# Kernel tuning notes

Hardware: AMD Instinct MI355X
Metric: run time of the kernel (lower is better)

## Reference

```python
import jax, jax.numpy as jnp
import numpy as np


def conv1x1(x, W, b):
    # 1x1 conv == channel mixing: [O,C] x [B,C,H,W] -> [B,O,H,W]
    return jnp.einsum('oc,bchw->bohw', W, x) + b[None, :, None, None]


def _fmm(x, x_th, Wk_rgb, bk_rgb, Wk_th, bk_th, Wv_rgb, bv_rgb, Wv_th, bv_th,
         gamma_rgb, gamma_th, gamma2_rgb, gamma2_th):
    b, c, w, h = x.shape
    n = w * h
    x_k    = conv1x1(x,    Wk_rgb, bk_rgb).reshape(b, c, n)
    x_th_k = conv1x1(x_th, Wk_th,  bk_th ).reshape(b, c, n)
    x_v    = conv1x1(x,    Wv_rgb, bv_rgb).reshape(b, c, n)
    x_v_th = conv1x1(x_th, Wv_th,  bv_th ).reshape(b, c, n)

    # spatial attention: sim[b, n, m] = x_th_k^T @ x_k, softmax over m
    sim = jax.nn.softmax(jnp.einsum('bcn,bcm->bnm', x_th_k, x_k), axis=-1)
    x_1    = jnp.einsum('bcn,bnm->bcm', x_v,    sim).reshape(b, c, w, h)
    x_th_1 = jnp.einsum('bcn,bnm->bcm', x_v_th, sim).reshape(b, c, w, h)
    x_1    = x_1 * gamma_rgb + x
    x_th_1 = x_th_1 * gamma_th + x_th

    # channel attention with max-subtraction (note: uses value projections, not x_1)
    energy = jnp.einsum('bcn,bdn->bcd', x_v_th, x_v)  # [b, c, c]
    sim_c = jax.nn.softmax(jnp.max(energy, axis=-1, keepdims=True) - energy, axis=-1)
    x_2    = jnp.einsum('bcd,bdn->bcn', sim_c, x_v   ).reshape(b, c, w, h)
    x_th_2 = jnp.einsum('bcd,bdn->bcn', sim_c, x_v_th).reshape(b, c, w, h)
    x_2    = gamma2_rgb * x_2    + x_1
    x_th_2 = gamma2_th  * x_th_2 + x_th_1
    return x_2, x_th_2


def setup_inputs() -> dict:
    key = jax.random.key(0)
    ks = jax.random.split(key, 12)
    b, c, w, h = 4, 256, 64, 64
    scale = 1.0 / np.sqrt(c)
    f32 = jnp.float32
    d = {
        'x':    jax.random.normal(ks[0], (b, c, w, h), f32),
        'x_th': jax.random.normal(ks[1], (b, c, w, h), f32),
        'Wk_rgb': jax.random.normal(ks[2], (c, c), f32) * scale,
        'bk_rgb': jax.random.normal(ks[3], (c,), f32) * 0.01,
        'Wk_th':  jax.random.normal(ks[4], (c, c), f32) * scale,
        'bk_th':  jax.random.normal(ks[5], (c,), f32) * 0.01,
        'Wv_rgb': jax.random.normal(ks[6], (c, c), f32) * scale,
        'bv_rgb': jax.random.normal(ks[7], (c,), f32) * 0.01,
        'Wv_th':  jax.random.normal(ks[8], (c, c), f32) * scale,
        'bv_th':  jax.random.normal(ks[9], (c,), f32) * 0.01,
        # gammas init to 0 in the original; use small nonzero so both branches are exercised
        'gamma_rgb':  jnp.full((1,), 0.5, f32),
        'gamma_th':   jnp.full((1,), 0.4, f32),
        'gamma2_rgb': jnp.full((1,), 0.3, f32),
        'gamma2_th':  jnp.full((1,), 0.2, f32),
    }
    return d


def reference(x, x_th, Wk_rgb, bk_rgb, Wk_th, bk_th, Wv_rgb, bv_rgb, Wv_th, bv_th,
              gamma_rgb, gamma_th, gamma2_rgb, gamma2_th):
    return _fmm(x, x_th, Wk_rgb, bk_rgb, Wk_th, bk_th, Wv_rgb, bv_rgb, Wv_th, bv_th,
                gamma_rgb, gamma_th, gamma2_rgb, gamma2_th)
```

## Files before the change

### kernel.cpp

```cpp
#include <hip/hip_runtime.h>

typedef unsigned short u16;
typedef unsigned int u32;
typedef __attribute__((ext_vector_type(8))) _Float16 f16x8;
typedef __attribute__((ext_vector_type(4))) float f32x4;

#define DEVINL __device__ __forceinline__
#define LOG2E 1.44269504f

DEVINL u16 f2h_u(float f) { _Float16 h = (_Float16)f; return __builtin_bit_cast(unsigned short, h); }
DEVINL float h2f_u(u16 h) { return (float)__builtin_bit_cast(_Float16, h); }
DEVINL float ex2(float x) { return __builtin_amdgcn_exp2f(x); }

DEVINL f16x8 ldfrag(const u16* p) {
    int4 d = *(const int4*)p;
    return __builtin_bit_cast(f16x8, d);
}

DEVINL void glds16(const u16* g, u16* l) {
    __builtin_amdgcn_global_load_lds(
        (const __attribute__((address_space(1))) unsigned int*)g,
        (__attribute__((address_space(3))) unsigned int*)l, 16, 0, 0);
}

#define CFENCE  asm volatile("" ::: "memory")
#define VMCNT8  asm volatile("s_waitcnt vmcnt(8)" ::: "memory")
#define VMCNT0  asm volatile("s_waitcnt vmcnt(0)" ::: "memory")
#define LGKM0   asm volatile("s_waitcnt lgkmcnt(0)" ::: "memory")

static const long CN  = 256L * 4096L;
static const long PtE = 4096L * 4096L;

DEVINL void gemm_core(const u16* __restrict__ Ag, int lda,
                      const u16* __restrict__ Bg, int ldb,
                      int kOff, int kLen, u16* As, u16* Bs, f32x4 (&acc)[4][4])
{
    int tid = threadIdx.x;
    int lane = tid & 63, w = tid >> 6;
    int wr = w >> 1, wc = w & 1;
    int kg = lane >> 4, rl = lane & 15;
    int l8 = lane >> 3, c8 = lane & 7;

    int srow = w * 32 + l8;
    int scol = (c8 ^ l8) * 8;
    const u16* aS = Ag + (size_t)srow * lda + kOff + scol;
    const u16* bS = Bg + (size_t)srow * ldb + kOff + scol;
    int dOff = w * 2048;

    int rl7 = rl & 7;
    int e0 = (kg ^ rl7) * 8;
    int e1 = e0 ^ 32;
    int aRow = (wr * 64 + rl) * 64;
    int bRow = (wc * 64 + rl) * 64;

    int nt = kLen >> 6;
#pragma unroll
    for (int q = 0; q < 4; ++q) {
        glds16(aS + (size_t)q * 8 * lda, As + dOff + q * 512);
        glds16(bS + (size_t)q * 8 * ldb, Bs + dOff + q * 512);
    }
#pragma unroll
    for (int q = 0; q < 4; ++q) {
        glds16(aS + (size_t)q * 8 * lda + 64, As + 8192 + dOff + q * 512);
        glds16(bS + (size_t)q * 8 * ldb + 64, Bs + 8192 + dOff + q * 512);
    }

    for (int t = 0; t < nt; ++t) {
        const u16* Ab = As + (t & 1) * 8192;
        const u16* Bb = Bs + (t & 1) * 8192;
        if (t + 1 < nt) { VMCNT8; } else { VMCNT0; }
        __builtin_amdgcn_s_barrier();
        CFENCE;
        f16x8 a0[4], b0[4], a1[4], b1[4];
#pragma unroll
        for (int i = 0; i < 4; ++i) a0[i] = ldfrag(&Ab[aRow + i * 1024 + e0]);
#pragma unroll
        for (int i = 0; i < 4; ++i) b0[i] = ldfrag(&Bb[bRow + i * 1024 + e0]);
#pragma unroll
        for (int i = 0; i < 4; ++i) a1[i] = ldfrag(&Ab[aRow + i * 1024 + e1]);
#pragma unroll
        for (int i = 0; i < 4; ++i) b1[i] = ldfrag(&Bb[bRow + i * 1024 + e1]);
        __builtin_amdgcn_s_setprio(1);
#pragma unroll
        for (int i = 0; i < 4; ++i)
#pragma unroll
            for (int j = 0; j < 4; ++j)
                acc[i][j] = __builtin_amdgcn_mfma_f32_16x16x32_f16(a0[i], b0[j], acc[i][j], 0, 0, 0);
#pragma unroll
        for (int i = 0; i < 4; ++i)
#pragma unroll
            for (int j = 0; j < 4; ++j)
                acc[i][j] = __builtin_amdgcn_mfma_f32_16x16x32_f16(a1[i], b1[j], acc[i][j], 0, 0, 0);
        __builtin_amdgcn_s_setprio(0);
        LGKM0;
        __builtin_amdgcn_s_barrier();
        CFENCE;
        if (t + 2 < nt) {
            const u16* aN = aS + (size_t)(t + 2) * 64;
            const u16* bN = bS + (size_t)(t + 2) * 64;
            u16* Ad = As + (t & 1) * 8192 + dOff;
            u16* Bd = Bs + (t & 1) * 8192 + dOff;
#pragma unroll
            for (int q = 0; q < 4; ++q) {
                glds16(aN + (size_t)q * 8 * lda, Ad + q * 512);
                glds16(bN + (size_t)q * 8 * ldb, Bd + q * 512);
            }
        }
    }
}

DEVINL void epi_f32_apply(f32x4 (&acc)[4][4], u16* AsRaw, int rowBase, int colBase,
                          float gamma, const float* __restrict__ src,
                          float* __restrict__ out)
{
    int tid = threadIdx.x;
    int lane = tid & 63, w = tid >> 6;
    int wr = w >> 1, wc = w & 1, kg = lane >> 4, rl = lane & 15;
    int rrow = lane & 15, rcg = lane >> 4;
    float* slab = (float*)AsRaw + w * 320;
#pragma unroll
    for (int i = 0; i < 4; ++i) {
        int row0 = rowBase + wr * 64 + i * 16;
#pragma unroll
        for (int j = 0; j < 4; ++j) {
            int col0 = colBase + wc * 64 + j * 16;
            f32x4 v = acc[i][j];
#pragma unroll
            for (int r = 0; r < 4; ++r) slab[(kg * 4 + r) * 20 + rl] = v[r];
            LGKM0;
            float4 vv = *(const float4*)(slab + rrow * 20 + rcg * 4);
            CFENCE;
            size_t o = (size_t)(row0 + rrow) * 4096 + col0 + rcg * 4;
            float4 sv = *(const float4*)(src + o);
            float4 ov;
            ov.x = gamma * vv.x + sv.x;
            ov.y = gamma * vv.y + sv.y;
            ov.z = gamma * vv.z + sv.z;
            ov.w = gamma * vv.w + sv.w;
            *(float4*)(out + o) = ov;
        }
    }
}

DEVINL void epi_f16_bias(f32x4 (&acc)[4][4], u16* AsRaw, int rowBase, int colBase,
                         int ldo, const float* __restrict__ bias, u16* __restrict__ out)
{
    int tid = threadIdx.x;
    int lane = tid & 63, w = tid >> 6;
    int wr = w >> 1, wc = w & 1, kg = lane >> 4, rl = lane & 15;
    int rrow = lane & 15, rcg = lane >> 4;
    float* slab = (float*)AsRaw + w * 320;
#pragma unroll
    for (int i = 0; i < 4; ++i) {
        int row0 = rowBase + wr * 64 + i * 16;
#pragma unroll
        for (int j = 0; j < 4; ++j) {
            int col0 = colBase + wc * 64 + j * 16;
            f32x4 v = acc[i][j];
#pragma unroll
            for (int r = 0; r < 4; ++r) slab[(kg * 4 + r) * 20 + rl] = v[r];
            LGKM0;
            float4 vv = *(const float4*)(slab + rrow * 20 + rcg * 4);
            CFENCE;
            float4 bb = *(const float4*)(bias + col0 + rcg * 4);
            u32 lo = (u32)f2h_u(vv.x + bb.x) | ((u32)f2h_u(vv.y + bb.y) << 16);
            u32 hi = (u32)f2h_u(vv.z + bb.z) | ((u32)f2h_u(vv.w + bb.w) << 16);
            uint2 pk; pk.x = lo; pk.y = hi;
            *(uint2*)(out + (size_t)(row0 + rrow) * ldo + col0 + rcg * 4) = pk;
        }
    }
}

DEVINL void mergeMS(float& m, float& s, float om, float os) {
    float nm = fmaxf(m, om);
    s = s * ex2((m - nm) * LOG2E) + os * ex2((om - nm) * LOG2E);
    m = nm;
}

__launch_bounds__(256, 2)
__global__ void st_gemm(const u16* __restrict__ Kt, const u16* __restrict__ Ktth,
                        u16* __restrict__ StH,
                        float* __restrict__ pmax, float* __restrict__ psum)
{
    __shared__ __align__(16) u16 As[2 * 8192];
    __shared__ __align__(16) u16 Bs[2 * 8192];
    int P = blockIdx.x;
    int L = (P & 7) * 512 + (P >> 3);
    int b = L >> 10, yb = (L >> 5) & 31, xb = L & 31;
    const u16* A = Kt   + (long)b * CN + (size_t)yb * 128 * 256;
    const u16* B = Ktth + (long)b * CN + (size_t)xb * 128 * 256;
    u16* out = StH + (long)b * PtE;
    int rowBase = yb * 128, colBase = xb * 128;

    f32x4 acc[4][4];
#pragma unroll
    for (int i = 0; i < 4; ++i)
#pragma unroll
        for (int j = 0; j < 4; ++j) acc[i][j] = (f32x4){0.f, 0.f, 0.f, 0.f};

    gemm_core(A, 256, B, 256, 0, 256, As, Bs, acc);

    int lane = threadIdx.x & 63, w = threadIdx.x >> 6;
    int wr = w >> 1, wc = w & 1, kg = lane >> 4, rl = lane & 15;
    int rrow = lane & 15, rcg = lane >> 4;
    float* slab = (float*)As + w * 320;

    float vr[4][4][4];
#pragma unroll
    for (int i = 0; i < 4; ++i) {
        int row0 = rowBase + wr * 64 + i * 16;
#pragma unroll
        for (int j = 0; j < 4; ++j) {
            int col0 = colBase + wc * 64 + j * 16;
            f32x4 v = acc[i][j];
#pragma unroll
            for (int r = 0; r < 4; ++r) {
                float xr = h2f_u(f2h_u(v[r]));
                vr[i][j][r] = xr;
                slab[(kg * 4 + r) * 20 + rl] = xr;
            }
            LGKM0;
            float4 vv = *(const float4*)(slab + rrow * 20 + rcg * 4);
            CFENCE;
            u32 lo = (u32)f2h_u(vv.x) | ((u32)f2h_u(vv.y) << 16);
            u32 hi = (u32)f2h_u(vv.z) | ((u32)f2h_u(vv.w) << 16);
            uint2 pk; pk.x = lo; pk.y = hi;
            *(uint2*)(out + (size_t)(row0 + rrow) * 4096 + col0 + rcg * 4) = pk;
        }
    }
    float tm[4], ts[4];
#pragma unroll
    for (int j = 0; j < 4; ++j) {
        float m = vr[0][j][0];
#pragma unroll
        for (int i = 0; i < 4; ++i)
#pragma unroll
            for (int r = 0; r < 4; ++r) m = fmaxf(m, vr[i][j][r]);
        float mk = m * LOG2E, s = 0.f;
#pragma unroll
        for (int i = 0; i < 4; ++i)
#pragma unroll
            for (int r = 0; r < 4; ++r) s += ex2(fmaf(vr[i][j][r], LOG2E, -mk));
        tm[j] = m; ts[j] = s;
    }
#pragma unroll
    for (int j = 0; j < 4; ++j) {
        mergeMS(tm[j], ts[j], __shfl_xor(tm[j], 16, 64), __shfl_xor(ts[j], 16, 64));
        mergeMS(tm[j], ts[j], __shfl_xor(tm[j], 32, 64), __shfl_xor(ts[j], 32, 64));
    }
    float* red = (float*)Bs;
    __syncthreads();
    if (wr == 1 && lane < 16) {
#pragma unroll
        for (int j = 0; j < 4; ++j) {
            red[((wc * 4 + j) * 16 + rl) * 2 + 0] = tm[j];
            red[((wc * 4 + j) * 16 + rl) * 2 + 1] = ts[j];
        }
    }
    __syncthreads();
    if (wr == 0 && lane < 16) {
#pragma unroll
        for (int j = 0; j < 4; ++j) {
            mergeMS(tm[j], ts[j], red[((wc * 4 + j) * 16 + rl) * 2 + 0],
                                  red[((wc * 4 + j) * 16 + rl) * 2 + 1]);
            int col = colBase + wc * 64 + j * 16 + rl;
            long idx = ((long)b * 32 + yb) * 4096 + col;
            pmax[idx] = tm[j];
            psum[idx] = ts[j];
        }
    }
}

__global__ void stats_combine(const float* __restrict__ pmax, const float* __restrict__ psum,
                              float* __restrict__ cmK, float* __restrict__ crcp)
{
    int b = blockIdx.y;
    int col = blockIdx.x * 256 + threadIdx.x;
    const float* pm = pmax + (long)b * 32 * 4096 + col;
    const float* ps = psum + (long)b * 32 * 4096 + col;
    float m = -3.0e38f, s = 0.f;
    for (int i = 0; i < 32; ++i) mergeMS(m, s, pm[i * 4096], ps[i * 4096]);
    cmK[b * 4096 + col] = m * LOG2E;
    crcp[b * 4096 + col] = 1.f / s;
}

__global__ void pt8_kernel(u16* St, const float* __restrict__ cmK,
                           const float* __restrict__ crcp)
{
    int b = blockIdx.z;
    St += (long)b * PtE;
    cmK += b * 4096; crcp += b * 4096;
    int m = blockIdx.y;
    int c0 = (blockIdx.x * 256 + threadIdx.x) * 8;
    size_t o = (size_t)m * 4096 + c0;
    f16x8 hv = __builtin_bit_cast(f16x8, *(const int4*)(St + o));
    union { u16 q[8]; int4 v; } pk;
#pragma unroll
    for (int j = 0; j < 8; ++j)
        pk.q[j] = f2h_u(ex2(fmaf((float)hv[j], LOG2E, -cmK[c0 + j])) * crcp[c0 + j]);
    *(int4*)(St + o) = pk.v;
}

__launch_bounds__(256, 2)
__global__ void pv_gemm(const u16* __restrict__ V2, const u16* __restrict__ Pt,
                        const float* __restrict__ g0p, const float* __restrict__ g1p,
                        const float* __restrict__ src0, const float* __restrict__ src1,
                        float* __restrict__ out0, float* __restrict__ out1)
{
    __shared__ __align__(16) u16 As[2 * 8192];
    __shared__ __align__(16) u16 Bs[2 * 8192];
    int P = blockIdx.x;
    int L = (P & 7) * 64 + (P >> 3);
    int b = L >> 7, n = (L >> 2) & 31, y = (L >> 1) & 1, t = L & 1;
    const u16* A = V2 + ((long)b * 2 + t) * CN;
    const u16* B = Pt + (long)b * PtE;
    int rowBase = y * 128, colBase = n * 128;

    f32x4 acc[4][4];
#pragma unroll
    for (int i = 0; i < 4; ++i)
#pragma unroll
        for (int j = 0; j < 4; ++j) acc[i][j] = (f32x4){0.f, 0.f, 0.f, 0.f};

    gemm_core(A + (size_t)rowBase * 4096, 4096, B + (size_t)colBase * 4096, 4096,
              0, 4096, As, Bs, acc);

    float gamma = t ? *g1p : *g0p;
    const float* src = (t ? src1 : src0) + (long)b * CN;
    float* out = (t ? out1 : out0) + (long)b * CN;
    epi_f32_apply(acc, As, rowBase, colBase, gamma, src, out);
}

__launch_bounds__(256, 2)
__global__ void gemm_splitk(const u16* __restrict__ A, int lda, long sAz,
                            const u16* __restrict__ B, int ldb, long sBz,
                            int splitK, int zshift,
                            float* __restrict__ outf, int ldo, long sOz)
{
    __shared__ __align__(16) u16 As[2 * 8192];
    __shared__ __align__(16) u16 Bs[2 * 8192];
    int z = blockIdx.z;
    int bq = z >> zshift, s = z & ((1 << zshift) - 1);
    int kOff = s * splitK;
    A += sAz * bq; B += sBz * bq;
    long zo = sOz * bq;
    int rowBase = blockIdx.y * 128, colBase = blockIdx.x * 128;
    f32x4 acc[4][4];
#pragma unroll
    for (int i = 0; i < 4; ++i)
#pragma unroll
        for (int j = 0; j < 4; ++j) acc[i][j] = (f32x4){0.f, 0.f, 0.f, 0.f};

    gemm_core(A + (size_t)rowBase * lda, lda, B + (size_t)colBase * ldb, ldb, kOff, splitK, As, Bs, acc);

    int lane = threadIdx.x & 63, w = threadIdx.x >> 6;
    int wr = w >> 1, wc = w & 1, kg = lane >> 4, rl = lane & 15;
#pragma unroll
    for (int i = 0; i < 4; ++i) {
        int row0 = rowBase + wr * 64 + i * 16 + kg * 4;
#pragma unroll
        for (int j = 0; j < 4; ++j) {
            int col = colBase + wc * 64 + j * 16 + rl;
            f32x4 v = acc[i][j];
#pragma unroll
            for (int r = 0; r < 4; ++r)
                atomicAdd(&outf[zo + (size_t)(row0 + r) * ldo + col], v[r]);
        }
    }
}

__launch_bounds__(256, 2)
__global__ void proj_all(const u16* __restrict__ xT, const u16* __restrict__ xthT,
                         const u16* __restrict__ wts,
                         const float* __restrict__ b0, const float* __restrict__ b1,
                         const float* __restrict__ b2, const float* __restrict__ b3,
                         u16* o0, u16* o1, u16* o2, u16* o3)
{
    __shared__ __align__(16) u16 As[2 * 8192];
    __shared__ __align__(16) u16 Bs[2 * 8192];
    int z = blockIdx.z, b = z >> 2, t = z & 3;
    const u16* A = ((t & 1) ? xthT : xT) + (long)b * CN;
    const u16* B = wts + t * 65536;
    u16* out = t == 0 ? o0 + (long)b * CN : t == 1 ? o1 + (long)b * CN
             : t == 2 ? o2 + (long)b * 2 * CN : o3 + (long)b * 2 * CN;
    int rowBase = blockIdx.y * 128, colBase = blockIdx.x * 128;
    f32x4 acc[4][4];
#pragma unroll
    for (int i = 0; i < 4; ++i)
#pragma unroll
        for (int j = 0; j < 4; ++j) acc[i][j] = (f32x4){0.f, 0.f, 0.f, 0.f};

    gemm_core(A + (size_t)rowBase * 256, 256, B + (size_t)colBase * 256, 256, 0, 256, As, Bs, acc);

    const float* bias = t == 0 ? b0 : t == 1 ? b1 : t == 2 ? b2 : b3;
    epi_f16_bias(acc, As, rowBase, colBase, 256, bias, out);
}

__launch_bounds__(256, 2)
__global__ void ch_gemm(const u16* __restrict__ simcb, const u16* __restrict__ Vt2,
                        const float* __restrict__ g0p, const float* __restrict__ g1p,
                        const float* __restrict__ src0, const float* __restrict__ src1,
                        float* __restrict__ out0, float* __restrict__ out1)
{
    __shared__ __align__(16) u16 As[2 * 8192];
    __shared__ __align__(16) u16 Bs[2 * 8192];
    int P = blockIdx.x;
    int L = (P & 7) * 64 + (P >> 3);
    int b = L >> 7, t = (L >> 6) & 1, n = (L >> 1) & 31, y = L & 1;
    const u16* A = simcb + (long)b * 65536;
    const u16* B = Vt2 + ((long)b * 2 + t) * CN;
    int rowBase = y * 128, colBase = n * 128;

    f32x4 acc[4][4];
#pragma unroll
    for (int i = 0; i < 4; ++i)
#pragma unroll
        for (int j = 0; j < 4; ++j) acc[i][j] = (f32x4){0.f, 0.f, 0.f, 0.f};

    gemm_core(A + (size_t)rowBase * 256, 256, B + (size_t)colBase * 256, 256, 0, 256, As, Bs, acc);

    float gamma = t ? *g1p : *g0p;
    const float* src = (t ? src1 : src0) + (long)b * CN;
    float* out = (t ? out1 : out0) + (long)b * CN;
    epi_f32_apply(acc, As, rowBase, colBase, gamma, src, out);
}

__global__ void tr_f32_h2(const float* __restrict__ in0, const float* __restrict__ in1,
                          u16* __restrict__ out0, u16* __restrict__ out1)
{
    int z = blockIdx.z, b = z & 3;
    const float* in = ((z >> 2) ? in1 : in0) + (long)b * CN;
    u16* out = ((z >> 2) ? out1 : out0) + (long)b * CN;
    __shared__ u16 s[64 * 65];
    int tx = threadIdx.x & 63, tw = threadIdx.x >> 6;
    int r0 = blockIdx.y * 64, c0 = blockIdx.x * 64;
#pragma unroll
    for (int p = 0; p < 16; ++p) {
        int r = tw + p * 4;
        s[tx * 65 + r] = f2h_u(in[(size_t)(r0 + r) * 4096 + c0 + tx]);
    }
    __syncthreads();
#pragma unroll
    for (int p = 0; p < 16; ++p) {
        int rr = tw + p * 4;
        out[(size_t)(c0 + rr) * 256 + r0 + tx] = s[rr * 65 + tx];
    }
}

__global__ void tr_h_h(const u16* __restrict__ in, u16* __restrict__ out,
                       int R, int NC_, long sIn, long sOut)
{
    in += (long)blockIdx.z * sIn; out += (long)blockIdx.z * sOut;
    __shared__ u16 s[64 * 65];
    int tx = threadIdx.x & 63, tw = threadIdx.x >> 6;
    int r0 = blockIdx.y * 64, c0 = blockIdx.x * 64;
#pragma unroll
    for (int p = 0; p < 16; ++p) {
        int r = tw + p * 4;
        s[tx * 65 + r] = in[(size_t)(r0 + r) * NC_ + c0 + tx];
    }
    __syncthreads();
#pragma unroll
    for (int p = 0; p < 16; ++p) {
        int rr = tw + p * 4;
        out[(size_t)(c0 + rr) * R + r0 + tx] = s[rr * 65 + tx];
    }
}

__global__ void cvt_w_kernel(const float* __restrict__ w0, const float* __restrict__ w1,
                             const float* __restrict__ w2, const float* __restrict__ w3,
                             u16* __restrict__ out)
{
    int i = blockIdx.x * 256 + threadIdx.x;
    const float* w = (i < 65536) ? w0 : (i < 131072) ? w1 : (i < 196608) ? w2 : w3;
    out[i] = f2h_u(w[i & 65535]);
}

DEVINL float blockReduce(float v, int op) {
    __shared__ float s[4];
#pragma unroll
    for (int o = 32; o; o >>= 1) {
        float t = __shfl_xor(v, o, 64);
        v = op ? (v + t) : fmaxf(v, t);
    }
    __syncthreads();
    if ((threadIdx.x & 63) == 0) s[threadIdx.x >> 6] = v;
    __syncthreads();
    return op ? (s[0] + s[1] + s[2] + s[3]) : fmaxf(fmaxf(s[0], s[1]), fmaxf(s[2], s[3]));
}

__global__ void simc_kernel(const float* __restrict__ E, u16* __restrict__ simc)
{
    int bb = blockIdx.y;
    const float* Eb = E + bb * 65536;
    u16* sc = simc + bb * 65536;
    int c = blockIdx.x, d = threadIdx.x;
    float e = Eb[c * 256 + d];
    float rmax = blockReduce(e, 0);
    float v = rmax - e;
    float vmax = blockReduce(v, 0);
    float p = __expf(v - vmax);
    float s = blockReduce(p, 1);
    sc[c * 256 + d] = f2h_u(p / s);
}

extern "C" void kernel_launch(void* const* d_in, const int* in_sizes, int n_in,
                              void* d_out, int out_size, void* d_ws, size_t ws_size,
                              hipStream_t stream)
{
    const float* x      = (const float*)d_in[0];
    const float* xth    = (const float*)d_in[1];
    const float* Wk_rgb = (const float*)d_in[2];
    const float* bk_rgb = (const float*)d_in[3];
    const float* Wk_th  = (const float*)d_in[4];
    const float* bk_th  = (const float*)d_in[5];
    const float* Wv_rgb = (const float*)d_in[6];
    const float* bv_rgb = (const float*)d_in[7];
    const float* Wv_th  = (const float*)d_in[8];
    const float* bv_th  = (const float*)d_in[9];
    const float* g1r = (const float*)d_in[10];
    const float* g1t = (const float*)d_in[11];
    const float* g2r = (const float*)d_in[12];
    const float* g2t = (const float*)d_in[13];

    u16* wts   = (u16*)d_ws;
    u16* Kt    = wts + 4 * 65536;
    u16* Ktth  = Kt + 4 * CN;
    u16* Vt2   = Ktth + 4 * CN;
    u16* V2    = Vt2 + 8 * CN;
    u16* StH   = V2 + 8 * CN;
    u16* simc   = Kt;
    float* E    = (float*)(Kt + 4 * 65536);
    float* cmK  = E + 4 * 65536;
    float* crcp = cmK + 4 * 4096;
    u16* xT    = StH;
    u16* xthT  = xT + 4 * CN;

    float* outX2  = (float*)d_out;
    float* outXt2 = outX2 + 4 * CN;

    float* pmax = outX2;
    float* psum = pmax + 4 * 32 * 4096;

    cvt_w_kernel<<<1024, 256, 0, stream>>>(Wk_rgb, Wk_th, Wv_rgb, Wv_th, wts);
    tr_f32_h2<<<dim3(64, 4, 8), 256, 0, stream>>>(x, xth, xT, xthT);

    proj_all<<<dim3(2, 32, 16), 256, 0, stream>>>(xT, xthT, wts,
        bk_rgb, bk_th, bv_rgb, bv_th, Kt, Ktth, Vt2, Vt2 + CN);

    tr_h_h<<<dim3(4, 64, 8), 256, 0, stream>>>(Vt2, V2, 4096, 256, CN, CN);

    st_gemm<<<4096, 256, 0, stream>>>(Kt, Ktth, StH, pmax, psum);
    stats_combine<<<dim3(16, 4), 256, 0, stream>>>(pmax, psum, cmK, crcp);
    pt8_kernel<<<dim3(2, 4096, 4), 256, 0, stream>>>(StH, cmK, crcp);

    pv_gemm<<<512, 256, 0, stream>>>(
        V2, StH, g1r, g1t, x, xth, outX2, outXt2);

    (void)hipMemsetAsync(E, 0, 4 * 65536 * sizeof(float), stream);
    gemm_splitk<<<dim3(2, 2, 128), 256, 0, stream>>>(
        V2 + CN, 4096, 2 * CN, V2, 4096, 2 * CN,
        128, 5, E, 256, 65536);
    simc_kernel<<<dim3(256, 4), 256, 0, stream>>>(E, simc);

    ch_gemm<<<512, 256, 0, stream>>>(
        simc, Vt2, g2r, g2t, outX2, outXt2, outX2, outXt2);
}
```

Measured before the change: 285.3 us.

## Load A fragments directly to registers and drop LDS-staged epilogues

```diff
diff --git a/kernel.cpp b/kernel.cpp
--- a/kernel.cpp
+++ b/kernel.cpp
@@ -16,6 +16,7 @@
     int4 d = *(const int4*)p;
     return __builtin_bit_cast(f16x8, d);
 }
+DEVINL f16x8 h8(int4 d) { return __builtin_bit_cast(f16x8, d); }
 
 DEVINL void glds16(const u16* g, u16* l) {
     __builtin_amdgcn_global_load_lds(
@@ -24,7 +25,7 @@
 }
 
 #define CFENCE  asm volatile("" ::: "memory")
-#define VMCNT8  asm volatile("s_waitcnt vmcnt(8)" ::: "memory")
+#define VMCNT4  asm volatile("s_waitcnt vmcnt(4)" ::: "memory")
 #define VMCNT0  asm volatile("s_waitcnt vmcnt(0)" ::: "memory")
 #define LGKM0   asm volatile("s_waitcnt lgkmcnt(0)" ::: "memory")
 
@@ -33,7 +34,7 @@
 
 DEVINL void gemm_core(const u16* __restrict__ Ag, int lda,
                       const u16* __restrict__ Bg, int ldb,
-                      int kOff, int kLen, u16* As, u16* Bs, f32x4 (&acc)[4][4])
+                      int kOff, int kLen, u16* Bs, f32x4 (&acc)[4][4])
 {
     int tid = threadIdx.x;
     int lane = tid & 63, w = tid >> 6;
@@ -43,130 +44,77 @@
 
     int srow = w * 32 + l8;
     int scol = (c8 ^ l8) * 8;
-    const u16* aS = Ag + (size_t)srow * lda + kOff + scol;
     const u16* bS = Bg + (size_t)srow * ldb + kOff + scol;
     int dOff = w * 2048;
 
     int rl7 = rl & 7;
     int e0 = (kg ^ rl7) * 8;
     int e1 = e0 ^ 32;
-    int aRow = (wr * 64 + rl) * 64;
     int bRow = (wc * 64 + rl) * 64;
 
+    const u16* aP[4];
+#pragma unroll
+    for (int i = 0; i < 4; ++i)
+        aP[i] = Ag + (size_t)(wr * 64 + i * 16 + rl) * lda + kOff + kg * 8;
+
+    int4 aR[2][8];
+
     int nt = kLen >> 6;
 #pragma unroll
-    for (int q = 0; q < 4; ++q) {
-        glds16(aS + (size_t)q * 8 * lda, As + dOff + q * 512);
+    for (int q = 0; q < 4; ++q)
         glds16(bS + (size_t)q * 8 * ldb, Bs + dOff + q * 512);
-    }
-#pragma unroll
-    for (int q = 0; q < 4; ++q) {
-        glds16(aS + (size_t)q * 8 * lda + 64, As + 8192 + dOff + q * 512);
+    CFENCE;
+#pragma unroll
+    for (int i = 0; i < 4; ++i) {
+        aR[0][i]     = *(const int4*)(aP[i]);
+        aR[0][i + 4] = *(const int4*)(aP[i] + 32);
+    }
+    CFENCE;
+#pragma unroll
+    for (int q = 0; q < 4; ++q)
         glds16(bS + (size_t)q * 8 * ldb + 64, Bs + 8192 + dOff + q * 512);
-    }
 
     for (int t = 0; t < nt; ++t) {
-        const u16* Ab = As + (t & 1) * 8192;
-        const u16* Bb = Bs + (t & 1) * 8192;
-        if (t + 1 < nt) { VMCNT8; } else { VMCNT0; }
+        if (t + 1 < nt) { VMCNT4; } else { VMCNT0; }
         __builtin_amdgcn_s_barrier();
         CFENCE;
-        f16x8 a0[4], b0[4], a1[4], b1[4];
-#pragma unroll
-        for (int i = 0; i < 4; ++i) a0[i] = ldfrag(&Ab[aRow + i * 1024 + e0]);
-#pragma unroll
-        for (int i = 0; i < 4; ++i) b0[i] = ldfrag(&Bb[bRow + i * 1024 + e0]);
-#pragma unroll
-        for (int i = 0; i < 4; ++i) a1[i] = ldfrag(&Ab[aRow + i * 1024 + e1]);
-#pragma unroll
-        for (int i = 0; i < 4; ++i) b1[i] = ldfrag(&Bb[bRow + i * 1024 + e1]);
+        if (t + 1 < nt) {
+            int nb = (t + 1) & 1;
+#pragma unroll
+            for (int i = 0; i < 4; ++i) {
+                aR[nb][i]     = *(const int4*)(aP[i] + (size_t)(t + 1) * 64);
+                aR[nb][i + 4] = *(const int4*)(aP[i] + (size_t)(t + 1) * 64 + 32);
+            }
+            CFENCE;
+        }
+        const u16* Bb = Bs + (t & 1) * 8192;
+        f16x8 b0[4], b1[4];
+#pragma unroll
+        for (int j = 0; j < 4; ++j) b0[j] = ldfrag(&Bb[bRow + j * 1024 + e0]);
+#pragma unroll
+        for (int j = 0; j < 4; ++j) b1[j] = ldfrag(&Bb[bRow + j * 1024 + e1]);
+        int cb = t & 1;
         __builtin_amdgcn_s_setprio(1);
 #pragma unroll
         for (int i = 0; i < 4; ++i)
 #pragma unroll
             for (int j = 0; j < 4; ++j)
-                acc[i][j] = __builtin_amdgcn_mfma_f32_16x16x32_f16(a0[i], b0[j], acc[i][j], 0, 0, 0);
+                acc[i][j] = __builtin_amdgcn_mfma_f32_16x16x32_f16(h8(aR[cb][i]), b0[j], acc[i][j], 0, 0, 0);
 #pragma unroll
         for (int i = 0; i < 4; ++i)
 #pragma unroll
             for (int j = 0; j < 4; ++j)
-                acc[i][j] = __builtin_amdgcn_mfma_f32_16x16x32_f16(a1[i], b1[j], acc[i][j], 0, 0, 0);
+                acc[i][j] = __builtin_amdgcn_mfma_f32_16x16x32_f16(h8(aR[cb][i + 4]), b1[j], acc[i][j], 0, 0, 0);
         __builtin_amdgcn_s_setprio(0);
         LGKM0;
         __builtin_amdgcn_s_barrier();
         CFENCE;
         if (t + 2 < nt) {
-            const u16* aN = aS + (size_t)(t + 2) * 64;
             const u16* bN = bS + (size_t)(t + 2) * 64;
-            u16* Ad = As + (t & 1) * 8192 + dOff;
             u16* Bd = Bs + (t & 1) * 8192 + dOff;
 #pragma unroll
-            for (int q = 0; q < 4; ++q) {
-                glds16(aN + (size_t)q * 8 * lda, Ad + q * 512);
+            for (int q = 0; q < 4; ++q)
                 glds16(bN + (size_t)q * 8 * ldb, Bd + q * 512);
-            }
-        }
-    }
-}
-
-DEVINL void epi_f32_apply(f32x4 (&acc)[4][4], u16* AsRaw, int rowBase, int colBase,
-                          float gamma, const float* __restrict__ src,
-                          float* __restrict__ out)
-{
-    int tid = threadIdx.x;
-    int lane = tid & 63, w = tid >> 6;
-    int wr = w >> 1, wc = w & 1, kg = lane >> 4, rl = lane & 15;
-    int rrow = lane & 15, rcg = lane >> 4;
-    float* slab = (float*)AsRaw + w * 320;
-#pragma unroll
-    for (int i = 0; i < 4; ++i) {
-        int row0 = rowBase + wr * 64 + i * 16;
-#pragma unroll
-        for (int j = 0; j < 4; ++j) {
-            int col0 = colBase + wc * 64 + j * 16;
-            f32x4 v = acc[i][j];
-#pragma unroll
-            for (int r = 0; r < 4; ++r) slab[(kg * 4 + r) * 20 + rl] = v[r];
-            LGKM0;
-            float4 vv = *(const float4*)(slab + rrow * 20 + rcg * 4);
-            CFENCE;
-            size_t o = (size_t)(row0 + rrow) * 4096 + col0 + rcg * 4;
-            float4 sv = *(const float4*)(src + o);
-            float4 ov;
-            ov.x = gamma * vv.x + sv.x;
-            ov.y = gamma * vv.y + sv.y;
-            ov.z = gamma * vv.z + sv.z;
-            ov.w = gamma * vv.w + sv.w;
-            *(float4*)(out + o) = ov;
-        }
-    }
-}
-
-DEVINL void epi_f16_bias(f32x4 (&acc)[4][4], u16* AsRaw, int rowBase, int colBase,
-                         int ldo, const float* __restrict__ bias, u16* __restrict__ out)
-{
-    int tid = threadIdx.x;
-    int lane = tid & 63, w = tid >> 6;
-    int wr = w >> 1, wc = w & 1, kg = lane >> 4, rl = lane & 15;
-    int rrow = lane & 15, rcg = lane >> 4;
-    float* slab = (float*)AsRaw + w * 320;
-#pragma unroll
-    for (int i = 0; i < 4; ++i) {
-        int row0 = rowBase + wr * 64 + i * 16;
-#pragma unroll
-        for (int j = 0; j < 4; ++j) {
-            int col0 = colBase + wc * 64 + j * 16;
-            f32x4 v = acc[i][j];
-#pragma unroll
-            for (int r = 0; r < 4; ++r) slab[(kg * 4 + r) * 20 + rl] = v[r];
-            LGKM0;
-            float4 vv = *(const float4*)(slab + rrow * 20 + rcg * 4);
-            CFENCE;
-            float4 bb = *(const float4*)(bias + col0 + rcg * 4);
-            u32 lo = (u32)f2h_u(vv.x + bb.x) | ((u32)f2h_u(vv.y + bb.y) << 16);
-            u32 hi = (u32)f2h_u(vv.z + bb.z) | ((u32)f2h_u(vv.w + bb.w) << 16);
-            uint2 pk; pk.x = lo; pk.y = hi;
-            *(uint2*)(out + (size_t)(row0 + rrow) * ldo + col0 + rcg * 4) = pk;
         }
     }
 }
@@ -182,7 +130,6 @@
                         u16* __restrict__ StH,
                         float* __restrict__ pmax, float* __restrict__ psum)
 {
-    __shared__ __align__(16) u16 As[2 * 8192];
     __shared__ __align__(16) u16 Bs[2 * 8192];
     int P = blockIdx.x;
     int L = (P & 7) * 512 + (P >> 3);
@@ -198,34 +145,25 @@
 #pragma unroll
         for (int j = 0; j < 4; ++j) acc[i][j] = (f32x4){0.f, 0.f, 0.f, 0.f};
 
-    gemm_core(A, 256, B, 256, 0, 256, As, Bs, acc);
+    gemm_core(A, 256, B, 256, 0, 256, Bs, acc);
 
     int lane = threadIdx.x & 63, w = threadIdx.x >> 6;
     int wr = w >> 1, wc = w & 1, kg = lane >> 4, rl = lane & 15;
-    int rrow = lane & 15, rcg = lane >> 4;
-    float* slab = (float*)As + w * 320;
 
     float vr[4][4][4];
 #pragma unroll
     for (int i = 0; i < 4; ++i) {
-        int row0 = rowBase + wr * 64 + i * 16;
-#pragma unroll
-        for (int j = 0; j < 4; ++j) {
-            int col0 = colBase + wc * 64 + j * 16;
+        int row0 = rowBase + wr * 64 + i * 16 + kg * 4;
+#pragma unroll
+        for (int j = 0; j < 4; ++j) {
+            int col = colBase + wc * 64 + j * 16 + rl;
             f32x4 v = acc[i][j];
 #pragma unroll
             for (int r = 0; r < 4; ++r) {
-                float xr = h2f_u(f2h_u(v[r]));
-                vr[i][j][r] = xr;
-                slab[(kg * 4 + r) * 20 + rl] = xr;
+                u16 h = f2h_u(v[r]);
+                out[(size_t)(row0 + r) * 4096 + col] = h;
+                vr[i][j][r] = h2f_u(h);
             }
-            LGKM0;
-            float4 vv = *(const float4*)(slab + rrow * 20 + rcg * 4);
-            CFENCE;
-            u32 lo = (u32)f2h_u(vv.x) | ((u32)f2h_u(vv.y) << 16);
-            u32 hi = (u32)f2h_u(vv.z) | ((u32)f2h_u(vv.w) << 16);
-            uint2 pk; pk.x = lo; pk.y = hi;
-            *(uint2*)(out + (size_t)(row0 + rrow) * 4096 + col0 + rcg * 4) = pk;
         }
     }
     float tm[4], ts[4];
@@ -307,7 +245,6 @@
                         const float* __restrict__ src0, const float* __restrict__ src1,
                         float* __restrict__ out0, float* __restrict__ out1)
 {
-    __shared__ __align__(16) u16 As[2 * 8192];
     __shared__ __align__(16) u16 Bs[2 * 8192];
     int P = blockIdx.x;
     int L = (P & 7) * 64 + (P >> 3);
@@ -323,12 +260,27 @@
         for (int j = 0; j < 4; ++j) acc[i][j] = (f32x4){0.f, 0.f, 0.f, 0.f};
 
     gemm_core(A + (size_t)rowBase * 4096, 4096, B + (size_t)colBase * 4096, 4096,
-              0, 4096, As, Bs, acc);
+              0, 4096, Bs, acc);
 
     float gamma = t ? *g1p : *g0p;
     const float* src = (t ? src1 : src0) + (long)b * CN;
     float* out = (t ? out1 : out0) + (long)b * CN;
-    epi_f32_apply(acc, As, rowBase, colBase, gamma, src, out);
+    int lane = threadIdx.x & 63, w = threadIdx.x >> 6;
+    int wr = w >> 1, wc = w & 1, kg = lane >> 4, rl = lane & 15;
+#pragma unroll
+    for (int i = 0; i < 4; ++i) {
+        int row0 = rowBase + wr * 64 + i * 16 + kg * 4;
+#pragma unroll
+        for (int j = 0; j < 4; ++j) {
+            int col = colBase + wc * 64 + j * 16 + rl;
+            f32x4 v = acc[i][j];
+#pragma unroll
+            for (int r = 0; r < 4; ++r) {
+                int row = row0 + r;
+                out[(size_t)row * 4096 + col] = gamma * v[r] + src[(size_t)row * 4096 + col];
+            }
+        }
+    }
 }
 
 __launch_bounds__(256, 2)
@@ -337,7 +289,6 @@
                             int splitK, int zshift,
                             float* __restrict__ outf, int ldo, long sOz)
 {
-    __shared__ __align__(16) u16 As[2 * 8192];
     __shared__ __align__(16) u16 Bs[2 * 8192];
     int z = blockIdx.z;
     int bq = z >> zshift, s = z & ((1 << zshift) - 1);
@@ -351,7 +302,7 @@
 #pragma unroll
         for (int j = 0; j < 4; ++j) acc[i][j] = (f32x4){0.f, 0.f, 0.f, 0.f};
 
-    gemm_core(A + (size_t)rowBase * lda, lda, B + (size_t)colBase * ldb, ldb, kOff, splitK, As, Bs, acc);
+    gemm_core(A + (size_t)rowBase * lda, lda, B + (size_t)colBase * ldb, ldb, kOff, splitK, Bs, acc);
 
     int lane = threadIdx.x & 63, w = threadIdx.x >> 6;
     int wr = w >> 1, wc = w & 1, kg = lane >> 4, rl = lane & 15;
@@ -376,7 +327,6 @@
                          const float* __restrict__ b2, const float* __restrict__ b3,
                          u16* o0, u16* o1, u16* o2, u16* o3)
 {
-    __shared__ __align__(16) u16 As[2 * 8192];
     __shared__ __align__(16) u16 Bs[2 * 8192];
     int z = blockIdx.z, b = z >> 2, t = z & 3;
     const u16* A = ((t & 1) ? xthT : xT) + (long)b * CN;
@@ -390,10 +340,23 @@
 #pragma unroll
         for (int j = 0; j < 4; ++j) acc[i][j] = (f32x4){0.f, 0.f, 0.f, 0.f};
 
-    gemm_core(A + (size_t)rowBase * 256, 256, B + (size_t)colBase * 256, 256, 0, 256, As, Bs, acc);
+    gemm_core(A + (size_t)rowBase * 256, 256, B + (size_t)colBase * 256, 256, 0, 256, Bs, acc);
 
     const float* bias = t == 0 ? b0 : t == 1 ? b1 : t == 2 ? b2 : b3;
-    epi_f16_bias(acc, As, rowBase, colBase, 256, bias, out);
+    int lane = threadIdx.x & 63, w = threadIdx.x >> 6;
+    int wr = w >> 1, wc = w & 1, kg = lane >> 4, rl = lane & 15;
+#pragma unroll
+    for (int i = 0; i < 4; ++i) {
+        int row0 = rowBase + wr * 64 + i * 16 + kg * 4;
+#pragma unroll
+        for (int j = 0; j < 4; ++j) {
+            int col = colBase + wc * 64 + j * 16 + rl;
+            f32x4 v = acc[i][j];
+#pragma unroll
+            for (int r = 0; r < 4; ++r)
+                out[(size_t)(row0 + r) * 256 + col] = f2h_u(v[r] + bias[col]);
+        }
+    }
 }
 
 __launch_bounds__(256, 2)
@@ -402,7 +365,6 @@
                         const float* __restrict__ src0, const float* __restrict__ src1,
                         float* __restrict__ out0, float* __restrict__ out1)
 {
-    __shared__ __align__(16) u16 As[2 * 8192];
     __shared__ __align__(16) u16 Bs[2 * 8192];
     int P = blockIdx.x;
     int L = (P & 7) * 64 + (P >> 3);
@@ -417,12 +379,27 @@
 #pragma unroll
         for (int j = 0; j < 4; ++j) acc[i][j] = (f32x4){0.f, 0.f, 0.f, 0.f};
 
-    gemm_core(A + (size_t)rowBase * 256, 256, B + (size_t)colBase * 256, 256, 0, 256, As, Bs, acc);
+    gemm_core(A + (size_t)rowBase * 256, 256, B + (size_t)colBase * 256, 256, 0, 256, Bs, acc);
 
     float gamma = t ? *g1p : *g0p;
     const float* src = (t ? src1 : src0) + (long)b * CN;
     float* out = (t ? out1 : out0) + (long)b * CN;
-    epi_f32_apply(acc, As, rowBase, colBase, gamma, src, out);
+    int lane = threadIdx.x & 63, w = threadIdx.x >> 6;
+    int wr = w >> 1, wc = w & 1, kg = lane >> 4, rl = lane & 15;
+#pragma unroll
+    for (int i = 0; i < 4; ++i) {
+        int row0 = rowBase + wr * 64 + i * 16 + kg * 4;
+#pragma unroll
+        for (int j = 0; j < 4; ++j) {
+            int col = colBase + wc * 64 + j * 16 + rl;
+            f32x4 v = acc[i][j];
+#pragma unroll
+            for (int r = 0; r < 4; ++r) {
+                int row = row0 + r;
+                out[(size_t)row * 4096 + col] = gamma * v[r] + src[(size_t)row * 4096 + col];
+            }
+        }
+    }
 }
 
 __global__ void tr_f32_h2(const float* __restrict__ in0, const float* __restrict__ in1,
```

Measured after the change: 639.7 us. +124.2%, slower.
